# Optimization experiments

Hardware: AMD Instinct MI355X
Metric: run time of the kernel (lower is better)

Reference implementation:

```python
import jax, jax.numpy as jnp
import numpy as np
from jax import lax

NVOX = 100
EPS = 1e-4
DN = ('NDHWC', 'DHWIO', 'NDHWC')

# scn semantics emulated densely: inactive voxels are identically zero and the
# active-site mask is re-applied after every layer, so submanifold convolution,
# strided sparse conv, sparse deconv and masked BN-ReLU compute the same values
# at active sites as SparseConvNet's rulebook gather-GEMM-scatter.

def _bnrelu(x, p, mask):
    # p: [4, C] = (gamma, beta, running_mean, running_var); inference-form BN.
    g, b, mu, v = p[0], p[1], p[2], p[3]
    return jax.nn.relu((x - mu) * (g * lax.rsqrt(v + EPS)) + b) * mask

def _subconv(x, w, mask):
    # Submanifold conv: inputs outside active set are zero; outputs only at active sites.
    return lax.conv_general_dilated(x, w, (1, 1, 1), 'SAME', dimension_numbers=DN) * mask

def _down(x, w):
    # scn.Convolution(dim, a, b, size=2, stride=2, bias=False)
    return lax.conv_general_dilated(x, w, (2, 2, 2), 'VALID', dimension_numbers=DN)

def _up(x, w, mask):
    # scn.Deconvolution restores the pre-downsample active set -> mask with finer mask.
    return lax.conv_transpose(x, w, (2, 2, 2), 'VALID', dimension_numbers=DN) * mask

def _pool_mask(mask):
    return lax.reduce_window(mask, 0.0, lax.max, (1, 2, 2, 2, 1), (1, 2, 2, 2, 1), 'VALID')

def _forward(coords, feats, w_in, w0a, wdown0, w1a, wdown1, w2, wup1, w1post, wup0, w0post,
             bnA, bnB, bnC, bnD, bnE, bnF, bnG, bnH, bnI, bnJ, linW, linb):
    i, j, k = coords[:, 0], coords[:, 1], coords[:, 2]
    # InputLayer mode=3: sum features at duplicate coordinates.
    grid = jnp.zeros((1, NVOX, NVOX, NVOX, 1), feats.dtype).at[0, i, j, k, 0].add(feats[:, 0])
    mask0 = jnp.zeros((1, NVOX, NVOX, NVOX, 1), feats.dtype).at[0, i, j, k, 0].set(1.0)
    mask1 = _pool_mask(mask0)   # 50^3 active set after strided conv
    mask2 = _pool_mask(mask1)   # 25^3

    x = _subconv(grid, w_in, mask0)                          # 1 -> 32
    x0 = _subconv(_bnrelu(x, bnA, mask0), w0a, mask0)        # level-0 VGG block
    d0 = _down(_bnrelu(x0, bnB, mask0), wdown0)              # 32 -> 64, 100 -> 50
    x1 = _subconv(_bnrelu(d0, bnC, mask1), w1a, mask1)       # level-1 VGG block
    d1 = _down(_bnrelu(x1, bnD, mask1), wdown1)              # 64 -> 96, 50 -> 25
    x2 = _subconv(_bnrelu(d1, bnE, mask2), w2, mask2)        # level-2 VGG block
    u1 = _up(_bnrelu(x2, bnF, mask2), wup1, mask1)           # 96 -> 64, 25 -> 50
    y1 = _subconv(_bnrelu(jnp.concatenate([x1, u1], -1), bnG, mask1), w1post, mask1)  # 128 -> 64
    u0 = _up(_bnrelu(y1, bnH, mask1), wup0, mask0)           # 64 -> 32, 50 -> 100
    y0 = _subconv(_bnrelu(jnp.concatenate([x0, u0], -1), bnI, mask0), w0post, mask0)  # 64 -> 32
    y = _bnrelu(y0, bnJ, mask0)                              # final BatchNormReLU(32)
    pts = y[0, i, j, k, :]                                   # OutputLayer: gather active sites [N,32]
    return pts @ linW + linb                                 # Linear(32, 3)


def setup_inputs() -> dict:
    key = jax.random.key(0)
    ks = jax.random.split(key, 24)
    N = 120000
    coords = jax.random.randint(ks[0], (N, 3), 0, NVOX, dtype=jnp.int32)
    feats = jax.random.normal(ks[1], (N, 1), jnp.float32)

    def w(k, shape, fan_in):
        return (jax.random.normal(k, shape, jnp.float32) / np.float32(np.sqrt(fan_in)))

    def bn(k, c):
        k1, k2, k3, k4 = jax.random.split(k, 4)
        return jnp.stack([
            1.0 + 0.1 * jax.random.normal(k1, (c,)),
            0.1 * jax.random.normal(k2, (c,)),
            0.1 * jax.random.normal(k3, (c,)),
            0.5 + jax.random.uniform(k4, (c,)),
        ]).astype(jnp.float32)

    return dict(
        coords=coords, feats=feats,
        w_in=w(ks[2], (3, 3, 3, 1, 32), 27),
        w0a=w(ks[3], (3, 3, 3, 32, 32), 27 * 32),
        wdown0=w(ks[4], (2, 2, 2, 32, 64), 8 * 32),
        w1a=w(ks[5], (3, 3, 3, 64, 64), 27 * 64),
        wdown1=w(ks[6], (2, 2, 2, 64, 96), 8 * 64),
        w2=w(ks[7], (3, 3, 3, 96, 96), 27 * 96),
        wup1=w(ks[8], (2, 2, 2, 96, 64), 96),
        w1post=w(ks[9], (3, 3, 3, 128, 64), 27 * 128),
        wup0=w(ks[10], (2, 2, 2, 64, 32), 64),
        w0post=w(ks[11], (3, 3, 3, 64, 32), 27 * 64),
        bnA=bn(ks[12], 32), bnB=bn(ks[13], 32), bnC=bn(ks[14], 64), bnD=bn(ks[15], 64),
        bnE=bn(ks[16], 96), bnF=bn(ks[17], 96), bnG=bn(ks[18], 128), bnH=bn(ks[19], 64),
        bnI=bn(ks[20], 64), bnJ=bn(ks[21], 32),
        linW=w(ks[22], (32, 3), 32),
        linb=0.01 * jax.random.normal(ks[23], (3,), jnp.float32),
    )


def reference(coords, feats, w_in, w0a, wdown0, w1a, wdown1, w2, wup1, w1post, wup0, w0post,
              bnA, bnB, bnC, bnD, bnE, bnF, bnG, bnH, bnI, bnJ, linW, linb):
    return _forward(coords, feats, w_in, w0a, wdown0, w1a, wdown1, w2, wup1, w1post, wup0, w0post,
                    bnA, bnB, bnC, bnD, bnE, bnF, bnG, bnH, bnI, bnJ, linW, linb)
```

## Files before the change

### kernel.cpp

```cpp
#include <hip/hip_runtime.h>


#define NVOX 100
#define EPSB 1e-4f
typedef unsigned long long u64;
typedef _Float16 h2 __attribute__((ext_vector_type(2)));
typedef _Float16 h8 __attribute__((ext_vector_type(8)));
typedef float f16v __attribute__((ext_vector_type(16)));
#define DEVFN __device__ __forceinline__

template<int NTAPS, int CTOT, int COUT>
__global__ __launch_bounds__(256)
void prepB32(const float* __restrict__ w, h2* __restrict__ out)
{
    constexpr int CTG = COUT / 32, KCH = CTOT / 16;
    const int n = NTAPS * CTG * KCH * 256;
    const int idx = blockIdx.x * 256 + threadIdx.x;
    if (idx >= n) return;
    const int jh = idx & 3;
    const int lane = (idx >> 2) & 63;
    int r = idx >> 8;
    const int kc = r % KCH; r /= KCH;
    const int ct = r % CTG; const int t = r / CTG;
    const int k0 = kc * 16 + (lane >> 5) * 8 + 2 * jh;
    const int co = ct * 32 + (lane & 31);
    h2 v;
    v[0] = (_Float16)w[((size_t)t * CTOT + k0) * COUT + co];
    v[1] = (_Float16)w[((size_t)t * CTOT + k0 + 1) * COUT + co];
    out[idx] = v;
}

template<int KC1, int KC2, int CTILES, int COUT, int S>
__global__ __launch_bounds__(64)
void gconv_m32(const h2* __restrict__ inA, const h2* __restrict__ inB,
               const h2* __restrict__ wb,
               const int* __restrict__ amap, const int* __restrict__ vlist,
               const int* __restrict__ cnt, int cap, float* __restrict__ out)
{
    constexpr int KCH = KC1 + KC2;
    constexpr int CTG = COUT / 32;
    const int lane = threadIdx.x;
    const int cntv = *cnt;
    const int wbase = blockIdx.x * 32;
    if (wbase >= cntv) return;
    const int ct0 = blockIdx.y * CTILES;
    const int l31 = lane & 31, ksub = lane >> 5;
    const int slot = wbase + l31;
    const bool on = slot < cntv;
    int X = 0, Y = 0, Z = 0;
    if (on) { const int v = vlist[slot]; X = v % S; const int r = v / S; Y = r % S; Z = r / S; }

    auto calc_ns = [&](int t) -> int {
        int ns = cap;
        if (on) {
            const int dz = t / 9 - 1, dy = (t / 3) % 3 - 1, dx = t % 3 - 1;
            const int nz = Z + dz, ny = Y + dy, nx = X + dx;
            if ((unsigned)nz < (unsigned)S && (unsigned)ny < (unsigned)S &&
                (unsigned)nx < (unsigned)S) {
                const int m = amap[(nz * S + ny) * S + nx];
                if (m >= 0) ns = m;
            }
        }
        return ns;
    };

    f16v acc[CTILES];
#pragma unroll
    for (int c = 0; c < CTILES; ++c) acc[c] = (f16v)(0.f);

    int ns = calc_ns(0);
#pragma unroll 1
    for (int t = 0; t < 27; ++t) {
        const int ns_nxt = (t + 1 < 27) ? calc_ns(t + 1) : cap;
        const h2* __restrict__ wt = wb + ((size_t)t * CTG + ct0) * KCH * 256;
#pragma unroll
        for (int kc = 0; kc < KC1; ++kc) {
            const h8 a = *reinterpret_cast<const h8*>(
                inA + (size_t)ns * (KC1 * 8) + kc * 8 + ksub * 4);
#pragma unroll
            for (int ct = 0; ct < CTILES; ++ct) {
                const h8 b = *reinterpret_cast<const h8*>(
                    wt + ((size_t)ct * KCH + kc) * 256 + lane * 4);
                acc[ct] = __builtin_amdgcn_mfma_f32_32x32x16_f16(a, b, acc[ct], 0, 0, 0);
            }
        }
        if constexpr (KC2 > 0) {
#pragma unroll
            for (int kc = 0; kc < KC2; ++kc) {
                const h8 a = *reinterpret_cast<const h8*>(
                    inB + (size_t)ns * (KC2 * 8) + kc * 8 + ksub * 4);
#pragma unroll
                for (int ct = 0; ct < CTILES; ++ct) {
                    const h8 b = *reinterpret_cast<const h8*>(
                        wt + ((size_t)ct * KCH + KC1 + kc) * 256 + lane * 4);
                    acc[ct] = __builtin_amdgcn_mfma_f32_32x32x16_f16(a, b, acc[ct], 0, 0, 0);
                }
            }
        }
        ns = ns_nxt;
    }
#pragma unroll
    for (int ct = 0; ct < CTILES; ++ct)
#pragma unroll
        for (int r = 0; r < 16; ++r) {
            const int row = (r & 3) + 8 * (r >> 2) + 4 * ksub;
            const int srow = wbase + row;
            if (srow < cntv)
                out[(size_t)srow * COUT + (ct0 + ct) * 32 + l31] = acc[ct][r];
        }
}

template<int KCH, int CTILES, int COUT, int SC>
__global__ __launch_bounds__(64)
void dconv_m32(const h2* __restrict__ in, const h2* __restrict__ wb,
               const int* __restrict__ amap_f, const int* __restrict__ vlist_c,
               const int* __restrict__ cnt_c, int capf, float* __restrict__ out)
{
    constexpr int SF = SC * 2;
    constexpr int CTG = COUT / 32;
    const int lane = threadIdx.x;
    const int cntv = *cnt_c;
    const int wbase = blockIdx.x * 32;
    if (wbase >= cntv) return;
    const int ct0 = blockIdx.y * CTILES;
    const int l31 = lane & 31, ksub = lane >> 5;
    const int slot = wbase + l31;
    const bool on = slot < cntv;
    int X = 0, Y = 0, Z = 0;
    if (on) { const int v = vlist_c[slot]; X = v % SC; const int r = v / SC; Y = r % SC; Z = r / SC; }

    auto calc_ns = [&](int t) -> int {
        int ns = capf;
        if (on) {
            const int fz = 2 * Z + ((t >> 2) & 1);
            const int fy = 2 * Y + ((t >> 1) & 1);
            const int fx = 2 * X + (t & 1);
            const int m = amap_f[(fz * SF + fy) * SF + fx];
            if (m >= 0) ns = m;
        }
        return ns;
    };

    f16v acc[CTILES];
#pragma unroll
    for (int c = 0; c < CTILES; ++c) acc[c] = (f16v)(0.f);

    int ns = calc_ns(0);
#pragma unroll 1
    for (int t = 0; t < 8; ++t) {
        const int ns_nxt = (t + 1 < 8) ? calc_ns(t + 1) : capf;
        const h2* __restrict__ wt = wb + ((size_t)t * CTG + ct0) * KCH * 256;
#pragma unroll
        for (int kc = 0; kc < KCH; ++kc) {
            const h8 a = *reinterpret_cast<const h8*>(
                in + (size_t)ns * (KCH * 8) + kc * 8 + ksub * 4);
#pragma unroll
            for (int ct = 0; ct < CTILES; ++ct) {
                const h8 b = *reinterpret_cast<const h8*>(
                    wt + ((size_t)ct * KCH + kc) * 256 + lane * 4);
                acc[ct] = __builtin_amdgcn_mfma_f32_32x32x16_f16(a, b, acc[ct], 0, 0, 0);
            }
        }
        ns = ns_nxt;
    }
#pragma unroll
    for (int ct = 0; ct < CTILES; ++ct)
#pragma unroll
        for (int r = 0; r < 16; ++r) {
            const int row = (r & 3) + 8 * (r >> 2) + 4 * ksub;
            const int srow = wbase + row;
            if (srow < cntv)
                out[(size_t)srow * COUT + (ct0 + ct) * 32 + l31] = acc[ct][r];
        }
}

__global__ __launch_bounds__(256)
void act_h16(const float* __restrict__ src, h2* __restrict__ dst,
             const float* __restrict__ sc, const float* __restrict__ sh,
             const int* __restrict__ cnt, int C)
{
    const int f = (blockIdx.x * 256 + threadIdx.x) * 8;
    if (f >= (*cnt) * C) return;
    const int c0 = f % C;
    const float4 v0 = *reinterpret_cast<const float4*>(src + f);
    const float4 v1 = *reinterpret_cast<const float4*>(src + f + 4);
    const float r[8] = {
        fmaxf(fmaf(v0.x, sc[c0 + 0], sh[c0 + 0]), 0.f),
        fmaxf(fmaf(v0.y, sc[c0 + 1], sh[c0 + 1]), 0.f),
        fmaxf(fmaf(v0.z, sc[c0 + 2], sh[c0 + 2]), 0.f),
        fmaxf(fmaf(v0.w, sc[c0 + 3], sh[c0 + 3]), 0.f),
        fmaxf(fmaf(v1.x, sc[c0 + 4], sh[c0 + 4]), 0.f),
        fmaxf(fmaf(v1.y, sc[c0 + 5], sh[c0 + 5]), 0.f),
        fmaxf(fmaf(v1.z, sc[c0 + 6], sh[c0 + 6]), 0.f),
        fmaxf(fmaf(v1.w, sc[c0 + 7], sh[c0 + 7]), 0.f)};
    union { float4 v; h2 h[4]; } o;
#pragma unroll
    for (int k = 0; k < 4; ++k) {
        h2 p; p[0] = (_Float16)r[2 * k]; p[1] = (_Float16)r[2 * k + 1];
        o.h[k] = p;
    }
    *reinterpret_cast<float4*>(dst + f / 2) = o.v;
}


template<int CTOT, int COUT>
DEVFN void stage_tap(const float* __restrict__ wtap, int cg32,
                     float* __restrict__ lbuf, int wid, int lane)
{
    constexpr int IPW = CTOT / 32;
#pragma unroll
    for (int i = 0; i < IPW; ++i) {
        const int chunk = wid * IPW + i;
        const int f4i = chunk * 64 + lane;
        const int ci = f4i >> 3, sub = f4i & 7;
        const float* g = wtap + ci * COUT + cg32 + sub * 4;
        __builtin_amdgcn_global_load_lds(
            (const __attribute__((address_space(1))) void*)g,
            (__attribute__((address_space(3))) void*)(lbuf + chunk * 256),
            16, 0, 0);
    }
}

template<int CIN>
DEVFN void dorow8(const float* __restrict__ row, const float* __restrict__ wl,
                  float (&acc)[8])
{
#pragma unroll 4
    for (int c0 = 0; c0 < CIN; c0 += 4) {
        const float4 a = *reinterpret_cast<const float4*>(row + c0);
        const float av[4] = {a.x, a.y, a.z, a.w};
#pragma unroll
        for (int j = 0; j < 4; ++j) {
            const float4 w0 = *reinterpret_cast<const float4*>(wl + (c0 + j) * 32);
            const float4 w1 = *reinterpret_cast<const float4*>(wl + (c0 + j) * 32 + 4);
            acc[0] = fmaf(av[j], w0.x, acc[0]);
            acc[1] = fmaf(av[j], w0.y, acc[1]);
            acc[2] = fmaf(av[j], w0.z, acc[2]);
            acc[3] = fmaf(av[j], w0.w, acc[3]);
            acc[4] = fmaf(av[j], w1.x, acc[4]);
            acc[5] = fmaf(av[j], w1.y, acc[5]);
            acc[6] = fmaf(av[j], w1.z, acc[6]);
            acc[7] = fmaf(av[j], w1.w, acc[7]);
        }
    }
}

template<int CIN, int COUT, int SC>
__global__ __launch_bounds__(256)
void uconv_w(const float* __restrict__ in, const float* __restrict__ w,
             const int* __restrict__ amap_f, const int* __restrict__ vlist_c,
             const int* __restrict__ cnt_c, float* __restrict__ out)
{
    constexpr int SF = SC * 2;
    __shared__ float lw[2][CIN * 32];
    const int tid = threadIdx.x, lane = tid & 63, wid = tid >> 6;
    const int cntv = *cnt_c;
    if (blockIdx.x * 64 >= cntv) return;
    const int slot = blockIdx.x * 64 + lane;
    const int cg32 = blockIdx.y * 32;
    const bool on = slot < cntv;
    int X = 0, Y = 0, Z = 0;
    if (on) { const int v = vlist_c[slot]; X = v % SC; const int r = v / SC; Y = r % SC; Z = r / SC; }
    stage_tap<CIN, COUT>(w + (size_t)7 * CIN * COUT, cg32, lw[0], wid, lane);
    __syncthreads();
#pragma unroll 1
    for (int t = 0; t < 8; ++t) {
        if (t + 1 < 8)
            stage_tap<CIN, COUT>(w + (size_t)(6 - t) * CIN * COUT, cg32,
                                 lw[(t + 1) & 1], wid, lane);
        int cs = -1;
        if (on) {
            const int fz = 2 * Z + ((t >> 2) & 1);
            const int fy = 2 * Y + ((t >> 1) & 1);
            const int fx = 2 * X + (t & 1);
            cs = amap_f[(fz * SF + fy) * SF + fx];
        }
        if (cs >= 0) {
            float acc[8];
#pragma unroll
            for (int q = 0; q < 8; ++q) acc[q] = 0.f;
            dorow8<CIN>(in + (size_t)slot * CIN, &lw[t & 1][wid * 8], acc);
            float* __restrict__ op = out + (size_t)cs * COUT + cg32 + wid * 8;
            *reinterpret_cast<float4*>(op) = make_float4(acc[0], acc[1], acc[2], acc[3]);
            *reinterpret_cast<float4*>(op + 4) = make_float4(acc[4], acc[5], acc[6], acc[7]);
        }
        __syncthreads();
    }
}

template<int OSPLIT, int S>
__global__ __launch_bounds__(64 * OSPLIT)
void cin_k(const float* __restrict__ grid, const float* __restrict__ w,
           const int* __restrict__ vlist, const int* __restrict__ cnt,
           float* __restrict__ out)
{
    constexpr int OW = 32 / OSPLIT;
    const int wOff = __builtin_amdgcn_readfirstlane(threadIdx.x >> 6) * OW;
    const int slot = blockIdx.x * 64 + (threadIdx.x & 63);
    if (slot >= *cnt) return;
    const int v = vlist[slot];
    const int x = v % S;
    const int rem = v / S;
    const int y = rem % S;
    const int z = rem / S;
    float acc[OW];
#pragma unroll
    for (int c = 0; c < OW; ++c) acc[c] = 0.f;
#pragma unroll
    for (int t = 0; t < 27; ++t) {
        const int dz = t / 9 - 1, dy = (t / 3) % 3 - 1, dx = t % 3 - 1;
        const int nz = z + dz, ny = y + dy, nx = x + dx;
        if ((unsigned)nz >= (unsigned)S || (unsigned)ny >= (unsigned)S ||
            (unsigned)nx >= (unsigned)S) continue;
        const float val = grid[(nz * S + ny) * S + nx];
        const float* __restrict__ wp = w + t * 32 + wOff;
#pragma unroll
        for (int c = 0; c < OW; ++c) acc[c] = fmaf(val, wp[c], acc[c]);
    }
    float* __restrict__ op = out + (size_t)slot * 32 + wOff;
#pragma unroll
    for (int c = 0; c < OW; ++c) op[c] = acc[c];
}

__global__ __launch_bounds__(256)
void act_k(const float* __restrict__ src, float* __restrict__ dst,
           const float* __restrict__ sc, const float* __restrict__ sh,
           const int* __restrict__ cnt, int C)
{
    const int f = (blockIdx.x * 256 + threadIdx.x) * 4;
    if (f >= (*cnt) * C) return;
    const int c0 = f % C;
    const float4 v = *reinterpret_cast<const float4*>(src + f);
    float4 o;
    o.x = fmaxf(fmaf(v.x, sc[c0 + 0], sh[c0 + 0]), 0.f);
    o.y = fmaxf(fmaf(v.y, sc[c0 + 1], sh[c0 + 1]), 0.f);
    o.z = fmaxf(fmaf(v.z, sc[c0 + 2], sh[c0 + 2]), 0.f);
    o.w = fmaxf(fmaf(v.w, sc[c0 + 3], sh[c0 + 3]), 0.f);
    *reinterpret_cast<float4*>(dst + f) = o;
}

__global__ __launch_bounds__(256)
void final_k(const int* __restrict__ coords, const float* __restrict__ y0,
             const int* __restrict__ amap0, const float* __restrict__ ssJ,
             const float* __restrict__ linW, const float* __restrict__ linb,
             int N, float* __restrict__ outp)
{
    const int n = blockIdx.x * blockDim.x + threadIdx.x;
    if (n >= N) return;
    const int i = coords[3 * n + 0];
    const int j = coords[3 * n + 1];
    const int k = coords[3 * n + 2];
    const int v = (i * NVOX + j) * NVOX + k;
    const int s = amap0[v];
    float a0 = linb[0], a1 = linb[1], a2 = linb[2];
    if (s >= 0) {
        const float* __restrict__ row = y0 + (size_t)s * 32;
#pragma unroll
        for (int c = 0; c < 32; ++c) {
            const float t = fmaxf(fmaf(row[c], ssJ[c], ssJ[32 + c]), 0.f);
            a0 = fmaf(t, linW[c * 3 + 0], a0);
            a1 = fmaf(t, linW[c * 3 + 1], a1);
            a2 = fmaf(t, linW[c * 3 + 2], a2);
        }
    }
    outp[3 * n + 0] = a0;
    outp[3 * n + 1] = a1;
    outp[3 * n + 2] = a2;
}

__global__ void bn_prep(const float* __restrict__ A, const float* __restrict__ B,
                        const float* __restrict__ C, const float* __restrict__ D,
                        const float* __restrict__ E, const float* __restrict__ F,
                        const float* __restrict__ G, const float* __restrict__ H,
                        const float* __restrict__ I, const float* __restrict__ J,
                        float* __restrict__ ss)
{
    const float* bp[10] = {A, B, C, D, E, F, G, H, I, J};
    const int CH[10] = {32, 32, 64, 64, 96, 96, 128, 64, 64, 32};
    int idx = blockIdx.x * blockDim.x + threadIdx.x;
    if (idx >= 672) return;
    int l = 0, base = 0, off2 = 0;
    while (idx >= base + CH[l]) { base += CH[l]; off2 += 2 * CH[l]; ++l; }
    const int c = idx - base;
    const float* bn = bp[l];
    const int Cc = CH[l];
    const float g = bn[c], b = bn[Cc + c], mu = bn[2 * Cc + c], var = bn[3 * Cc + c];
    const float sc = g * rsqrtf(var + EPSB);
    ss[off2 + c] = sc;
    ss[off2 + Cc + c] = b - mu * sc;
}

__global__ __launch_bounds__(256)
void scatter_mark(const int* __restrict__ coords, const float* __restrict__ feats,
                  int N, float* __restrict__ grid, int* __restrict__ amap0)
{
    const int n = blockIdx.x * blockDim.x + threadIdx.x;
    if (n >= N) return;
    const int i = coords[3 * n + 0];
    const int j = coords[3 * n + 1];
    const int k = coords[3 * n + 2];
    const int v = (i * NVOX + j) * NVOX + k;
    atomicAdd(&grid[v], feats[n]);
    amap0[v] = -2;
}

template<int SC>
__global__ __launch_bounds__(256)
void flag_coarse(const int* __restrict__ amap_f, int* __restrict__ amap_c)
{
    constexpr int SF = SC * 2;
    const int v = blockIdx.x * blockDim.x + threadIdx.x;
    if (v >= SC * SC * SC) return;
    const int x = v % SC;
    const int rem = v / SC;
    const int y = rem % SC;
    const int z = rem / SC;
    bool any = false;
#pragma unroll
    for (int t = 0; t < 8; ++t) {
        const int fz = 2 * z + ((t >> 2) & 1);
        const int fy = 2 * y + ((t >> 1) & 1);
        const int fx = 2 * x + (t & 1);
        if (amap_f[(fz * SF + fy) * SF + fx] >= 0) any = true;
    }
    amap_c[v] = any ? -2 : -1;
}

__global__ __launch_bounds__(256)
void count_k(const int* __restrict__ flags, int V, int* __restrict__ counts)
{
    const int v = blockIdx.x * 256 + threadIdx.x;
    const bool act = (v < V) && (flags[v] == -2);
    const u64 m = __ballot(act);
    __shared__ int c[4];
    const int wid = threadIdx.x >> 6;
    if ((threadIdx.x & 63) == 0) c[wid] = __popcll(m);
    __syncthreads();
    if (threadIdx.x == 0) counts[blockIdx.x] = c[0] + c[1] + c[2] + c[3];
}

__global__ __launch_bounds__(1024)
void scan_k(int* __restrict__ counts, int nb, int* __restrict__ total)
{
    __shared__ int sums[1024];
    const int t = threadIdx.x;
    int v[4];
    int s = 0;
#pragma unroll
    for (int i = 0; i < 4; ++i) {
        const int idx = t * 4 + i;
        v[i] = (idx < nb) ? counts[idx] : 0;
        s += v[i];
    }
    sums[t] = s;
    __syncthreads();
    for (int d = 1; d < 1024; d <<= 1) {
        const int add = (t >= d) ? sums[t - d] : 0;
        __syncthreads();
        sums[t] += add;
        __syncthreads();
    }
    int base = (t > 0) ? sums[t - 1] : 0;
#pragma unroll
    for (int i = 0; i < 4; ++i) {
        const int idx = t * 4 + i;
        if (idx < nb) counts[idx] = base;
        base += v[i];
    }
    if (t == 1023) *total = sums[1023];
}

__global__ __launch_bounds__(256)
void emit_k(int* __restrict__ amap, int V, const int* __restrict__ offsets,
            int* __restrict__ vlist)
{
    const int v = blockIdx.x * 256 + threadIdx.x;
    const bool act = (v < V) && (amap[v] == -2);
    const u64 m = __ballot(act);
    __shared__ int wbase[4];
    const int wid = threadIdx.x >> 6;
    const int lane = threadIdx.x & 63;
    if (lane == 0) wbase[wid] = __popcll(m);
    __syncthreads();
    if (threadIdx.x == 0) {
        int s = 0;
#pragma unroll
        for (int i = 0; i < 4; ++i) { const int t = wbase[i]; wbase[i] = s; s += t; }
    }
    __syncthreads();
    if (act) {
        const int slot = offsets[blockIdx.x] + wbase[wid] +
                         __popcll(m & ((1ull << lane) - 1ull));
        amap[v] = slot;
        vlist[slot] = v;
    }
}

extern "C" void kernel_launch(void* const* d_in, const int* in_sizes, int n_in,
                              void* d_out, int out_size, void* d_ws, size_t ws_size,
                              hipStream_t stream) {
    const int*   coords = (const int*)d_in[0];
    const float* feats  = (const float*)d_in[1];
    const float* w_in   = (const float*)d_in[2];
    const float* w0a    = (const float*)d_in[3];
    const float* wdown0 = (const float*)d_in[4];
    const float* w1a    = (const float*)d_in[5];
    const float* wdown1 = (const float*)d_in[6];
    const float* w2     = (const float*)d_in[7];
    const float* wup1   = (const float*)d_in[8];
    const float* w1post = (const float*)d_in[9];
    const float* wup0   = (const float*)d_in[10];
    const float* w0post = (const float*)d_in[11];
    const float* linW = (const float*)d_in[22];
    const float* linb = (const float*)d_in[23];
    float* outp = (float*)d_out;

    const int N = in_sizes[1];
    const int V0 = NVOX * NVOX * NVOX;
    const int V1 = 50 * 50 * 50;
    const int V2 = 25 * 25 * 25;
    const int cap0 = N;
    const int cap1 = 100000;
    const int cap2 = V2;

    char* ws = (char*)d_ws;
    size_t off = 0;
    auto alloc = [&](size_t bytes) -> void* {
        void* p = ws + off;
        off += (bytes + 255) & ~(size_t)255;
        return p;
    };
    int*   amap0  = (int*)alloc((size_t)V0 * 4);
    int*   vlist0 = (int*)alloc((size_t)cap0 * 4);
    int*   amap1  = (int*)alloc((size_t)V1 * 4);
    int*   vlist1 = (int*)alloc((size_t)cap1 * 4);
    int*   amap2  = (int*)alloc((size_t)V2 * 4);
    int*   vlist2 = (int*)alloc((size_t)cap2 * 4);
    int*   cnt    = (int*)alloc(3 * 4);
    int*   counts = (int*)alloc(4096 * 4);
    float* ss     = (float*)alloc(1344 * 4);
    float* grid   = (float*)alloc((size_t)V0 * 4);
    float* P1 = (float*)alloc((size_t)cap0 * 32 * 4);
    float* P2 = (float*)alloc((size_t)cap0 * 32 * 4);
    float* P3 = (float*)alloc((size_t)cap0 * 32 * 4);
    float* Q1 = (float*)alloc((size_t)cap1 * 64 * 4);
    float* Q2 = (float*)alloc((size_t)cap1 * 64 * 4);
    float* Q3 = (float*)alloc((size_t)cap1 * 64 * 4);
    float* R1 = (float*)alloc((size_t)cap2 * 96 * 4);
    float* R2 = (float*)alloc((size_t)cap2 * 96 * 4);
    h2* wbA  = (h2*)alloc((size_t)27 * 1 * 2 * 256 * 4);
    h2* wb1  = (h2*)alloc((size_t)27 * 2 * 4 * 256 * 4);
    h2* wb2  = (h2*)alloc((size_t)27 * 3 * 6 * 256 * 4);
    h2* wbP1 = (h2*)alloc((size_t)27 * 2 * 8 * 256 * 4);
    h2* wbP0 = (h2*)alloc((size_t)27 * 1 * 4 * 256 * 4);
    h2* wbD0 = (h2*)alloc((size_t)8 * 2 * 2 * 256 * 4);
    h2* wbD1 = (h2*)alloc((size_t)8 * 3 * 4 * 256 * 4);
    if (off > ws_size) return;

    h2* HA  = (h2*)P3;
    h2* HB  = (h2*)P3;
    h2* HC  = (h2*)Q3;
    h2* HD  = (h2*)Q3;
    h2* HE  = (h2*)Q1;
    h2* HG1 = (h2*)Q3;
    h2* HG2 = (h2*)P1;
    h2* HI1 = (h2*)P3;
    h2* HI2 = (h2*)Q2;

    const int B = 256;
    const int gN  = (N + B - 1) / B;
    const int nb0 = (V0 + B - 1) / B;
    const int nb1 = (V1 + B - 1) / B;
    const int nb2 = (V2 + B - 1) / B;
    const int gA64 = (cap1 * 64 / 4 + 255) / 256;
    const int gA96 = (cap2 * 96 / 4 + 255) / 256;
    const int gH32_0 = (cap0 * 32 / 8 + 255) / 256;
    const int gH64_1 = (cap1 * 64 / 8 + 255) / 256;
    const int gH96_2 = (cap2 * 96 / 8 + 255) / 256;
    const int sb0 = (cap0 + 63) / 64;
    const int sb1 = (cap1 + 63) / 64;
    const int sb2 = (cap2 + 63) / 64;
    const int g1w_0 = (cap0 + 31) / 32;
    const int g1w_1 = (cap1 + 31) / 32;
    const int g1w_2 = (cap2 + 31) / 32;

    hipMemsetAsync(amap0, 0xFF, (size_t)V0 * 4, stream);
    hipMemsetAsync(grid, 0, (size_t)V0 * 4, stream);
    bn_prep<<<3, 256, 0, stream>>>((const float*)d_in[12], (const float*)d_in[13],
                                   (const float*)d_in[14], (const float*)d_in[15],
                                   (const float*)d_in[16], (const float*)d_in[17],
                                   (const float*)d_in[18], (const float*)d_in[19],
                                   (const float*)d_in[20], (const float*)d_in[21], ss);
    prepB32<27, 32, 32><<<(27 * 1 * 2 * 256 + 255) / 256, 256, 0, stream>>>(w0a, wbA);
    prepB32<27, 64, 64><<<(27 * 2 * 4 * 256 + 255) / 256, 256, 0, stream>>>(w1a, wb1);
    prepB32<27, 96, 96><<<(27 * 3 * 6 * 256 + 255) / 256, 256, 0, stream>>>(w2, wb2);
    prepB32<27, 128, 64><<<(27 * 2 * 8 * 256 + 255) / 256, 256, 0, stream>>>(w1post, wbP1);
    prepB32<27, 64, 32><<<(27 * 1 * 4 * 256 + 255) / 256, 256, 0, stream>>>(w0post, wbP0);
    prepB32<8, 32, 64><<<(8 * 2 * 2 * 256 + 255) / 256, 256, 0, stream>>>(wdown0, wbD0);
    prepB32<8, 64, 96><<<(8 * 3 * 4 * 256 + 255) / 256, 256, 0, stream>>>(wdown1, wbD1);
    scatter_mark<<<gN, B, 0, stream>>>(coords, feats, N, grid, amap0);
    count_k<<<nb0, B, 0, stream>>>(amap0, V0, counts);
    scan_k<<<1, 1024, 0, stream>>>(counts, nb0, cnt + 0);
    emit_k<<<nb0, B, 0, stream>>>(amap0, V0, counts, vlist0);
    flag_coarse<50><<<nb1, B, 0, stream>>>(amap0, amap1);
    count_k<<<nb1, B, 0, stream>>>(amap1, V1, counts);
    scan_k<<<1, 1024, 0, stream>>>(counts, nb1, cnt + 1);
    emit_k<<<nb1, B, 0, stream>>>(amap1, V1, counts, vlist1);
    flag_coarse<25><<<nb2, B, 0, stream>>>(amap1, amap2);
    count_k<<<nb2, B, 0, stream>>>(amap2, V2, counts);
    scan_k<<<1, 1024, 0, stream>>>(counts, nb2, cnt + 2);
    emit_k<<<nb2, B, 0, stream>>>(amap2, V2, counts, vlist2);

    cin_k<2, 100><<<sb0, 128, 0, stream>>>(grid, w_in, vlist0, cnt + 0, P1);
    act_h16<<<gH32_0, 256, 0, stream>>>(P1, HA, ss + 0, ss + 32, cnt + 0, 32);
    hipMemsetAsync(HA + (size_t)cap0 * 16, 0, 16 * 4, stream);
    gconv_m32<2, 0, 1, 32, 100><<<dim3(g1w_0, 1), 64, 0, stream>>>(
        HA, nullptr, wbA, amap0, vlist0, cnt + 0, cap0, P2);
    act_h16<<<gH32_0, 256, 0, stream>>>(P2, HB, ss + 64, ss + 96, cnt + 0, 32);
    dconv_m32<2, 2, 64, 50><<<dim3(g1w_1, 1), 64, 0, stream>>>(
        HB, wbD0, amap0, vlist1, cnt + 1, cap0, Q1);
    act_h16<<<gH64_1, 256, 0, stream>>>(Q1, HC, ss + 128, ss + 192, cnt + 1, 64);
    hipMemsetAsync(HC + (size_t)cap1 * 32, 0, 32 * 4, stream);
    gconv_m32<4, 0, 2, 64, 50><<<dim3(g1w_1, 1), 64, 0, stream>>>(
        HC, nullptr, wb1, amap1, vlist1, cnt + 1, cap1, Q2);
    act_h16<<<gH64_1, 256, 0, stream>>>(Q2, HD, ss + 256, ss + 320, cnt + 1, 64);
    dconv_m32<4, 1, 96, 25><<<dim3(g1w_2, 3), 64, 0, stream>>>(
        HD, wbD1, amap1, vlist2, cnt + 2, cap1, R1);
    act_h16<<<gH96_2, 256, 0, stream>>>(R1, HE, ss + 384, ss + 480, cnt + 2, 96);
    hipMemsetAsync(HE + (size_t)cap2 * 48, 0, 48 * 4, stream);
    gconv_m32<6, 0, 1, 96, 25><<<dim3(g1w_2, 3), 64, 0, stream>>>(
        HE, nullptr, wb2, amap2, vlist2, cnt + 2, cap2, R2);
    act_k<<<gA96, 256, 0, stream>>>(R2, R2, ss + 576, ss + 672, cnt + 2, 96);
    uconv_w<96, 64, 25><<<dim3(sb2, 2), 256, 0, stream>>>(
        R2, wup1, amap1, vlist2, cnt + 2, Q1);
    act_h16<<<gH64_1, 256, 0, stream>>>(Q2, HG1, ss + 768, ss + 896, cnt + 1, 64);
    hipMemsetAsync(HG1 + (size_t)cap1 * 32, 0, 32 * 4, stream);
    act_h16<<<gH64_1, 256, 0, stream>>>(Q1, HG2, ss + 768 + 64, ss + 896 + 64, cnt + 1, 64);
    hipMemsetAsync(HG2 + (size_t)cap1 * 32, 0, 32 * 4, stream);
    gconv_m32<4, 4, 2, 64, 50><<<dim3(g1w_1, 1), 64, 0, stream>>>(
        HG1, HG2, wbP1, amap1, vlist1, cnt + 1, cap1, Q2);
    act_k<<<gA64, 256, 0, stream>>>(Q2, Q2, ss + 1024, ss + 1088, cnt + 1, 64);
    uconv_w<64, 32, 50><<<dim3(sb1, 1), 256, 0, stream>>>(
        Q2, wup0, amap0, vlist1, cnt + 1, P1);
    act_h16<<<gH32_0, 256, 0, stream>>>(P2, HI1, ss + 1152, ss + 1216, cnt + 0, 32);
    hipMemsetAsync(HI1 + (size_t)cap0 * 16, 0, 16 * 4, stream);
    act_h16<<<gH32_0, 256, 0, stream>>>(P1, HI2, ss + 1152 + 32, ss + 1216 + 32, cnt + 0, 32);
    hipMemsetAsync(HI2 + (size_t)cap0 * 16, 0, 16 * 4, stream);
    gconv_m32<2, 2, 1, 32, 100><<<dim3(g1w_0, 1), 64, 0, stream>>>(
        HI1, HI2, wbP0, amap0, vlist0, cnt + 0, cap0, P2);
    final_k<<<gN, B, 0, stream>>>(coords, P2, amap0, ss + 1280, linW, linb, N, outp);
}
```

Before: 515.8 us.

## Fuse BN-ReLU and fp16 conversion into conv epilogues, drop activation kernels

Folds the inference BatchNorm+ReLU and half-precision conversion into the epilogues of the sparse conv, downsample, upsample and input-conv kernels. Each conv output is written straight as the fp16 activation buffer the next layer reads, or as two differently normalized buffers when a skip connection needs one. This removes the separate act_h16/act_k passes and the fp32 intermediate round trips through memory, and moves the padding-row memsets to the start. Gconv/dconv now use one 32-channel tile per block with more blocks along y, trading weight reuse per block for parallelism. The epilogue now writes scattered 2-byte stores instead of vectorized ones.

```diff
diff --git a/kernel.cpp b/kernel.cpp
--- a/kernel.cpp
+++ b/kernel.cpp
@@ -8,6 +8,8 @@
 typedef _Float16 h8 __attribute__((ext_vector_type(8)));
 typedef float f16v __attribute__((ext_vector_type(16)));
 #define DEVFN __device__ __forceinline__
+
+DEVFN float bnr(float v, float sc, float sh) { return fmaxf(fmaf(v, sc, sh), 0.f); }
 
 template<int NTAPS, int CTOT, int COUT>
 __global__ __launch_bounds__(256)
@@ -30,12 +32,32 @@
     out[idx] = v;
 }
 
-template<int KC1, int KC2, int CTILES, int COUT, int S>
+template<int EMODE, int COUT>
+DEVFN void epilogue(float a, int srow, int ch,
+                    float* outF, _Float16* o1, const float* sc1, const float* sh1,
+                    _Float16* o2, const float* sc2, const float* sh2)
+{
+    if constexpr (EMODE == 0) {
+        outF[(size_t)srow * COUT + ch] = a;
+    } else if constexpr (EMODE == 3) {
+        outF[(size_t)srow * COUT + ch] = bnr(a, sc1[ch], sh1[ch]);
+    } else {
+        o1[(size_t)srow * COUT + ch] = (_Float16)bnr(a, sc1[ch], sh1[ch]);
+        if constexpr (EMODE == 2)
+            o2[(size_t)srow * COUT + ch] = (_Float16)bnr(a, sc2[ch], sh2[ch]);
+    }
+}
+
+template<int KC1, int KC2, int COUT, int S, int EMODE>
 __global__ __launch_bounds__(64)
 void gconv_m32(const h2* __restrict__ inA, const h2* __restrict__ inB,
                const h2* __restrict__ wb,
                const int* __restrict__ amap, const int* __restrict__ vlist,
-               const int* __restrict__ cnt, int cap, float* __restrict__ out)
+               const int* __restrict__ cnt, int cap,
+               float* __restrict__ outF, _Float16* __restrict__ o1,
+               const float* __restrict__ sc1, const float* __restrict__ sh1,
+               _Float16* __restrict__ o2,
+               const float* __restrict__ sc2, const float* __restrict__ sh2)
 {
     constexpr int KCH = KC1 + KC2;
     constexpr int CTG = COUT / 32;
@@ -43,7 +65,7 @@
     const int cntv = *cnt;
     const int wbase = blockIdx.x * 32;
     if (wbase >= cntv) return;
-    const int ct0 = blockIdx.y * CTILES;
+    const int ct0 = blockIdx.y;
     const int l31 = lane & 31, ksub = lane >> 5;
     const int slot = wbase + l31;
     const bool on = slot < cntv;
@@ -64,10 +86,7 @@
         return ns;
     };
 
-    f16v acc[CTILES];
-#pragma unroll
-    for (int c = 0; c < CTILES; ++c) acc[c] = (f16v)(0.f);
-
+    f16v acc = (f16v)(0.f);
     int ns = calc_ns(0);
 #pragma unroll 1
     for (int t = 0; t < 27; ++t) {
@@ -77,44 +96,39 @@
         for (int kc = 0; kc < KC1; ++kc) {
             const h8 a = *reinterpret_cast<const h8*>(
                 inA + (size_t)ns * (KC1 * 8) + kc * 8 + ksub * 4);
-#pragma unroll
-            for (int ct = 0; ct < CTILES; ++ct) {
-                const h8 b = *reinterpret_cast<const h8*>(
-                    wt + ((size_t)ct * KCH + kc) * 256 + lane * 4);
-                acc[ct] = __builtin_amdgcn_mfma_f32_32x32x16_f16(a, b, acc[ct], 0, 0, 0);
-            }
+            const h8 b = *reinterpret_cast<const h8*>(
+                wt + (size_t)kc * 256 + lane * 4);
+            acc = __builtin_amdgcn_mfma_f32_32x32x16_f16(a, b, acc, 0, 0, 0);
         }
         if constexpr (KC2 > 0) {
 #pragma unroll
             for (int kc = 0; kc < KC2; ++kc) {
                 const h8 a = *reinterpret_cast<const h8*>(
                     inB + (size_t)ns * (KC2 * 8) + kc * 8 + ksub * 4);
-#pragma unroll
-                for (int ct = 0; ct < CTILES; ++ct) {
-                    const h8 b = *reinterpret_cast<const h8*>(
-                        wt + ((size_t)ct * KCH + KC1 + kc) * 256 + lane * 4);
-                    acc[ct] = __builtin_amdgcn_mfma_f32_32x32x16_f16(a, b, acc[ct], 0, 0, 0);
-                }
+                const h8 b = *reinterpret_cast<const h8*>(
+                    wt + (size_t)(KC1 + kc) * 256 + lane * 4);
+                acc = __builtin_amdgcn_mfma_f32_32x32x16_f16(a, b, acc, 0, 0, 0);
             }
         }
         ns = ns_nxt;
     }
-#pragma unroll
-    for (int ct = 0; ct < CTILES; ++ct)
-#pragma unroll
-        for (int r = 0; r < 16; ++r) {
-            const int row = (r & 3) + 8 * (r >> 2) + 4 * ksub;
-            const int srow = wbase + row;
-            if (srow < cntv)
-                out[(size_t)srow * COUT + (ct0 + ct) * 32 + l31] = acc[ct][r];
-        }
-}
-
-template<int KCH, int CTILES, int COUT, int SC>
+    const int ch = ct0 * 32 + l31;
+#pragma unroll
+    for (int r = 0; r < 16; ++r) {
+        const int row = (r & 3) + 8 * (r >> 2) + 4 * ksub;
+        const int srow = wbase + row;
+        if (srow < cntv)
+            epilogue<EMODE, COUT>(acc[r], srow, ch, outF, o1, sc1, sh1, o2, sc2, sh2);
+    }
+}
+
+template<int KCH, int COUT, int SC, int EMODE>
 __global__ __launch_bounds__(64)
 void dconv_m32(const h2* __restrict__ in, const h2* __restrict__ wb,
                const int* __restrict__ amap_f, const int* __restrict__ vlist_c,
-               const int* __restrict__ cnt_c, int capf, float* __restrict__ out)
+               const int* __restrict__ cnt_c, int capf,
+               float* __restrict__ outF, _Float16* __restrict__ o1,
+               const float* __restrict__ sc1, const float* __restrict__ sh1)
 {
     constexpr int SF = SC * 2;
     constexpr int CTG = COUT / 32;
@@ -122,7 +136,7 @@
     const int cntv = *cnt_c;
     const int wbase = blockIdx.x * 32;
     if (wbase >= cntv) return;
-    const int ct0 = blockIdx.y * CTILES;
+    const int ct0 = blockIdx.y;
     const int l31 = lane & 31, ksub = lane >> 5;
     const int slot = wbase + l31;
     const bool on = slot < cntv;
@@ -141,10 +155,7 @@
         return ns;
     };
 
-    f16v acc[CTILES];
-#pragma unroll
-    for (int c = 0; c < CTILES; ++c) acc[c] = (f16v)(0.f);
-
+    f16v acc = (f16v)(0.f);
     int ns = calc_ns(0);
 #pragma unroll 1
     for (int t = 0; t < 8; ++t) {
@@ -154,52 +165,21 @@
         for (int kc = 0; kc < KCH; ++kc) {
             const h8 a = *reinterpret_cast<const h8*>(
                 in + (size_t)ns * (KCH * 8) + kc * 8 + ksub * 4);
-#pragma unroll
-            for (int ct = 0; ct < CTILES; ++ct) {
-                const h8 b = *reinterpret_cast<const h8*>(
-                    wt + ((size_t)ct * KCH + kc) * 256 + lane * 4);
-                acc[ct] = __builtin_amdgcn_mfma_f32_32x32x16_f16(a, b, acc[ct], 0, 0, 0);
-            }
+            const h8 b = *reinterpret_cast<const h8*>(
+                wt + (size_t)kc * 256 + lane * 4);
+            acc = __builtin_amdgcn_mfma_f32_32x32x16_f16(a, b, acc, 0, 0, 0);
         }
         ns = ns_nxt;
     }
-#pragma unroll
-    for (int ct = 0; ct < CTILES; ++ct)
-#pragma unroll
-        for (int r = 0; r < 16; ++r) {
-            const int row = (r & 3) + 8 * (r >> 2) + 4 * ksub;
-            const int srow = wbase + row;
-            if (srow < cntv)
-                out[(size_t)srow * COUT + (ct0 + ct) * 32 + l31] = acc[ct][r];
-        }
-}
-
-__global__ __launch_bounds__(256)
-void act_h16(const float* __restrict__ src, h2* __restrict__ dst,
-             const float* __restrict__ sc, const float* __restrict__ sh,
-             const int* __restrict__ cnt, int C)
-{
-    const int f = (blockIdx.x * 256 + threadIdx.x) * 8;
-    if (f >= (*cnt) * C) return;
-    const int c0 = f % C;
-    const float4 v0 = *reinterpret_cast<const float4*>(src + f);
-    const float4 v1 = *reinterpret_cast<const float4*>(src + f + 4);
-    const float r[8] = {
-        fmaxf(fmaf(v0.x, sc[c0 + 0], sh[c0 + 0]), 0.f),
-        fmaxf(fmaf(v0.y, sc[c0 + 1], sh[c0 + 1]), 0.f),
-        fmaxf(fmaf(v0.z, sc[c0 + 2], sh[c0 + 2]), 0.f),
-        fmaxf(fmaf(v0.w, sc[c0 + 3], sh[c0 + 3]), 0.f),
-        fmaxf(fmaf(v1.x, sc[c0 + 4], sh[c0 + 4]), 0.f),
-        fmaxf(fmaf(v1.y, sc[c0 + 5], sh[c0 + 5]), 0.f),
-        fmaxf(fmaf(v1.z, sc[c0 + 6], sh[c0 + 6]), 0.f),
-        fmaxf(fmaf(v1.w, sc[c0 + 7], sh[c0 + 7]), 0.f)};
-    union { float4 v; h2 h[4]; } o;
-#pragma unroll
-    for (int k = 0; k < 4; ++k) {
-        h2 p; p[0] = (_Float16)r[2 * k]; p[1] = (_Float16)r[2 * k + 1];
-        o.h[k] = p;
-    }
-    *reinterpret_cast<float4*>(dst + f / 2) = o.v;
+    const int ch = ct0 * 32 + l31;
+#pragma unroll
+    for (int r = 0; r < 16; ++r) {
+        const int row = (r & 3) + 8 * (r >> 2) + 4 * ksub;
+        const int srow = wbase + row;
+        if (srow < cntv)
+            epilogue<EMODE, COUT>(acc[r], srow, ch, outF, o1, sc1, sh1,
+                                  nullptr, nullptr, nullptr);
+    }
 }
 
 
@@ -249,7 +229,8 @@
 __global__ __launch_bounds__(256)
 void uconv_w(const float* __restrict__ in, const float* __restrict__ w,
              const int* __restrict__ amap_f, const int* __restrict__ vlist_c,
-             const int* __restrict__ cnt_c, float* __restrict__ out)
+             const int* __restrict__ cnt_c, _Float16* __restrict__ out,
+             const float* __restrict__ sc, const float* __restrict__ sh)
 {
     constexpr int SF = SC * 2;
     __shared__ float lw[2][CIN * 32];
@@ -280,22 +261,25 @@
 #pragma unroll
             for (int q = 0; q < 8; ++q) acc[q] = 0.f;
             dorow8<CIN>(in + (size_t)slot * CIN, &lw[t & 1][wid * 8], acc);
-            float* __restrict__ op = out + (size_t)cs * COUT + cg32 + wid * 8;
-            *reinterpret_cast<float4*>(op) = make_float4(acc[0], acc[1], acc[2], acc[3]);
-            *reinterpret_cast<float4*>(op + 4) = make_float4(acc[4], acc[5], acc[6], acc[7]);
+            union { float4 v[1]; _Float16 h[8]; } o;
+            const int chb = cg32 + wid * 8;
+#pragma unroll
+            for (int q = 0; q < 8; ++q)
+                o.h[q] = (_Float16)bnr(acc[q], sc[chb + q], sh[chb + q]);
+            *reinterpret_cast<float4*>(out + (size_t)cs * COUT + chb) = o.v[0];
         }
         __syncthreads();
     }
 }
 
-template<int OSPLIT, int S>
-__global__ __launch_bounds__(64 * OSPLIT)
+template<int S>
+__global__ __launch_bounds__(128)
 void cin_k(const float* __restrict__ grid, const float* __restrict__ w,
            const int* __restrict__ vlist, const int* __restrict__ cnt,
-           float* __restrict__ out)
-{
-    constexpr int OW = 32 / OSPLIT;
-    const int wOff = __builtin_amdgcn_readfirstlane(threadIdx.x >> 6) * OW;
+           _Float16* __restrict__ out, const float* __restrict__ sc,
+           const float* __restrict__ sh)
+{
+    const int wOff = __builtin_amdgcn_readfirstlane(threadIdx.x >> 6) * 16;
     const int slot = blockIdx.x * 64 + (threadIdx.x & 63);
     if (slot >= *cnt) return;
     const int v = vlist[slot];
@@ -303,9 +287,9 @@
     const int rem = v / S;
     const int y = rem % S;
     const int z = rem / S;
-    float acc[OW];
-#pragma unroll
-    for (int c = 0; c < OW; ++c) acc[c] = 0.f;
+    float acc[16];
+#pragma unroll
+    for (int c = 0; c < 16; ++c) acc[c] = 0.f;
 #pragma unroll
     for (int t = 0; t < 27; ++t) {
         const int dz = t / 9 - 1, dy = (t / 3) % 3 - 1, dx = t % 3 - 1;
@@ -315,28 +299,15 @@
         const float val = grid[(nz * S + ny) * S + nx];
         const float* __restrict__ wp = w + t * 32 + wOff;
 #pragma unroll
-        for (int c = 0; c < OW; ++c) acc[c] = fmaf(val, wp[c], acc[c]);
-    }
-    float* __restrict__ op = out + (size_t)slot * 32 + wOff;
-#pragma unroll
-    for (int c = 0; c < OW; ++c) op[c] = acc[c];
-}
-
-__global__ __launch_bounds__(256)
-void act_k(const float* __restrict__ src, float* __restrict__ dst,
-           const float* __restrict__ sc, const float* __restrict__ sh,
-           const int* __restrict__ cnt, int C)
-{
-    const int f = (blockIdx.x * 256 + threadIdx.x) * 4;
-    if (f >= (*cnt) * C) return;
-    const int c0 = f % C;
-    const float4 v = *reinterpret_cast<const float4*>(src + f);
-    float4 o;
-    o.x = fmaxf(fmaf(v.x, sc[c0 + 0], sh[c0 + 0]), 0.f);
-    o.y = fmaxf(fmaf(v.y, sc[c0 + 1], sh[c0 + 1]), 0.f);
-    o.z = fmaxf(fmaf(v.z, sc[c0 + 2], sh[c0 + 2]), 0.f);
-    o.w = fmaxf(fmaf(v.w, sc[c0 + 3], sh[c0 + 3]), 0.f);
-    *reinterpret_cast<float4*>(dst + f) = o;
+        for (int c = 0; c < 16; ++c) acc[c] = fmaf(val, wp[c], acc[c]);
+    }
+    union { float4 v[2]; _Float16 h[16]; } o;
+#pragma unroll
+    for (int c = 0; c < 16; ++c)
+        o.h[c] = (_Float16)bnr(acc[c], sc[wOff + c], sh[wOff + c]);
+    float4* dst = reinterpret_cast<float4*>(out + (size_t)slot * 32 + wOff);
+    dst[0] = o.v[0];
+    dst[1] = o.v[1];
 }
 
 __global__ __launch_bounds__(256)
@@ -357,7 +328,7 @@
         const float* __restrict__ row = y0 + (size_t)s * 32;
 #pragma unroll
         for (int c = 0; c < 32; ++c) {
-            const float t = fmaxf(fmaf(row[c], ssJ[c], ssJ[32 + c]), 0.f);
+            const float t = bnr(row[c], ssJ[c], ssJ[32 + c]);
             a0 = fmaf(t, linW[c * 3 + 0], a0);
             a1 = fmaf(t, linW[c * 3 + 1], a1);
             a2 = fmaf(t, linW[c * 3 + 2], a2);
@@ -540,14 +511,18 @@
     int*   counts = (int*)alloc(4096 * 4);
     float* ss     = (float*)alloc(1344 * 4);
     float* grid   = (float*)alloc((size_t)V0 * 4);
-    float* P1 = (float*)alloc((size_t)cap0 * 32 * 4);
-    float* P2 = (float*)alloc((size_t)cap0 * 32 * 4);
-    float* P3 = (float*)alloc((size_t)cap0 * 32 * 4);
-    float* Q1 = (float*)alloc((size_t)cap1 * 64 * 4);
-    float* Q2 = (float*)alloc((size_t)cap1 * 64 * 4);
-    float* Q3 = (float*)alloc((size_t)cap1 * 64 * 4);
-    float* R1 = (float*)alloc((size_t)cap2 * 96 * 4);
-    float* R2 = (float*)alloc((size_t)cap2 * 96 * 4);
+    _Float16* HA  = (_Float16*)alloc((size_t)(cap0 + 1) * 32 * 2);
+    _Float16* HB  = (_Float16*)alloc((size_t)(cap0 + 1) * 32 * 2);
+    _Float16* HI1 = (_Float16*)alloc((size_t)(cap0 + 1) * 32 * 2);
+    _Float16* HI2 = (_Float16*)alloc((size_t)(cap0 + 1) * 32 * 2);
+    _Float16* HC  = (_Float16*)alloc((size_t)(cap1 + 1) * 64 * 2);
+    _Float16* HD  = (_Float16*)alloc((size_t)(cap1 + 1) * 64 * 2);
+    _Float16* HG1 = (_Float16*)alloc((size_t)(cap1 + 1) * 64 * 2);
+    _Float16* HG2 = (_Float16*)alloc((size_t)(cap1 + 1) * 64 * 2);
+    _Float16* HE  = (_Float16*)alloc((size_t)(cap2 + 1) * 96 * 2);
+    float* y0f  = (float*)alloc((size_t)cap0 * 32 * 4);
+    float* actF = (float*)alloc((size_t)cap2 * 96 * 4);
+    float* actH = (float*)alloc((size_t)cap1 * 64 * 4);
     h2* wbA  = (h2*)alloc((size_t)27 * 1 * 2 * 256 * 4);
     h2* wb1  = (h2*)alloc((size_t)27 * 2 * 4 * 256 * 4);
     h2* wb2  = (h2*)alloc((size_t)27 * 3 * 6 * 256 * 4);
@@ -557,26 +532,11 @@
     h2* wbD1 = (h2*)alloc((size_t)8 * 3 * 4 * 256 * 4);
     if (off > ws_size) return;
 
-    h2* HA  = (h2*)P3;
-    h2* HB  = (h2*)P3;
-    h2* HC  = (h2*)Q3;
-    h2* HD  = (h2*)Q3;
-    h2* HE  = (h2*)Q1;
-    h2* HG1 = (h2*)Q3;
-    h2* HG2 = (h2*)P1;
-    h2* HI1 = (h2*)P3;
-    h2* HI2 = (h2*)Q2;
-
     const int B = 256;
     const int gN  = (N + B - 1) / B;
     const int nb0 = (V0 + B - 1) / B;
     const int nb1 = (V1 + B - 1) / B;
     const int nb2 = (V2 + B - 1) / B;
-    const int gA64 = (cap1 * 64 / 4 + 255) / 256;
-    const int gA96 = (cap2 * 96 / 4 + 255) / 256;
-    const int gH32_0 = (cap0 * 32 / 8 + 255) / 256;
-    const int gH64_1 = (cap1 * 64 / 8 + 255) / 256;
-    const int gH96_2 = (cap2 * 96 / 8 + 255) / 256;
     const int sb0 = (cap0 + 63) / 64;
     const int sb1 = (cap1 + 63) / 64;
     const int sb2 = (cap2 + 63) / 64;
@@ -586,6 +546,15 @@
 
     hipMemsetAsync(amap0, 0xFF, (size_t)V0 * 4, stream);
     hipMemsetAsync(grid, 0, (size_t)V0 * 4, stream);
+    hipMemsetAsync(HA + (size_t)cap0 * 32, 0, 64, stream);
+    hipMemsetAsync(HB + (size_t)cap0 * 32, 0, 64, stream);
+    hipMemsetAsync(HI1 + (size_t)cap0 * 32, 0, 64, stream);
+    hipMemsetAsync(HI2 + (size_t)cap0 * 32, 0, 64, stream);
+    hipMemsetAsync(HC + (size_t)cap1 * 64, 0, 128, stream);
+    hipMemsetAsync(HD + (size_t)cap1 * 64, 0, 128, stream);
+    hipMemsetAsync(HG1 + (size_t)cap1 * 64, 0, 128, stream);
+    hipMemsetAsync(HG2 + (size_t)cap1 * 64, 0, 128, stream);
+    hipMemsetAsync(HE + (size_t)cap2 * 96, 0, 192, stream);
     bn_prep<<<3, 256, 0, stream>>>((const float*)d_in[12], (const float*)d_in[13],
                                    (const float*)d_in[14], (const float*)d_in[15],
                                    (const float*)d_in[16], (const float*)d_in[17],
@@ -611,42 +580,32 @@
     scan_k<<<1, 1024, 0, stream>>>(counts, nb2, cnt + 2);
     emit_k<<<nb2, B, 0, stream>>>(amap2, V2, counts, vlist2);
 
-    cin_k<2, 100><<<sb0, 128, 0, stream>>>(grid, w_in, vlist0, cnt + 0, P1);
-    act_h16<<<gH32_0, 256, 0, stream>>>(P1, HA, ss + 0, ss + 32, cnt + 0, 32);
-    hipMemsetAsync(HA + (size_t)cap0 * 16, 0, 16 * 4, stream);
-    gconv_m32<2, 0, 1, 32, 100><<<dim3(g1w_0, 1), 64, 0, stream>>>(
-        HA, nullptr, wbA, amap0, vlist0, cnt + 0, cap0, P2);
-    act_h16<<<gH32_0, 256, 0, stream>>>(P2, HB, ss + 64, ss + 96, cnt + 0, 32);
-    dconv_m32<2, 2, 64, 50><<<dim3(g1w_1, 1), 64, 0, stream>>>(
-        HB, wbD0, amap0, vlist1, cnt + 1, cap0, Q1);
-    act_h16<<<gH64_1, 256, 0, stream>>>(Q1, HC, ss + 128, ss + 192, cnt + 1, 64);
-    hipMemsetAsync(HC + (size_t)cap1 * 32, 0, 32 * 4, stream);
-    gconv_m32<4, 0, 2, 64, 50><<<dim3(g1w_1, 1), 64, 0, stream>>>(
-        HC, nullptr, wb1, amap1, vlist1, cnt + 1, cap1, Q2);
-    act_h16<<<gH64_1, 256, 0, stream>>>(Q2, HD, ss + 256, ss + 320, cnt + 1, 64);
-    dconv_m32<4, 1, 96, 25><<<dim3(g1w_2, 3), 64, 0, stream>>>(
-        HD, wbD1, amap1, vlist2, cnt + 2, cap1, R1);
-    act_h16<<<gH96_2, 256, 0, stream>>>(R1, HE, ss + 384, ss + 480, cnt + 2, 96);
-    hipMemsetAsync(HE + (size_t)cap2 * 48, 0, 48 * 4, stream);
-    gconv_m32<6, 0, 1, 96, 25><<<dim3(g1w_2, 3), 64, 0, stream>>>(
-        HE, nullptr, wb2, amap2, vlist2, cnt + 2, cap2, R2);
-    act_k<<<gA96, 256, 0, stream>>>(R2, R2, ss + 576, ss + 672, cnt + 2, 96);
+    cin_k<100><<<sb0, 128, 0, stream>>>(grid, w_in, vlist0, cnt + 0, HA,
+                                        ss + 0, ss + 32);
+    gconv_m32<2, 0, 32, 100, 2><<<dim3(g1w_0, 1), 64, 0, stream>>>(
+        (const h2*)HA, nullptr, wbA, amap0, vlist0, cnt + 0, cap0,
+        nullptr, HB, ss + 64, ss + 96, HI1, ss + 1152, ss + 1216);
+    dconv_m32<2, 64, 50, 1><<<dim3(g1w_1, 2), 64, 0, stream>>>(
+        (const h2*)HB, wbD0, amap0, vlist1, cnt + 1, cap0,
+        nullptr, HC, ss + 128, ss + 192);
+    gconv_m32<4, 0, 64, 50, 2><<<dim3(g1w_1, 2), 64, 0, stream>>>(
+        (const h2*)HC, nullptr, wb1, amap1, vlist1, cnt + 1, cap1,
+        nullptr, HD, ss + 256, ss + 320, HG1, ss + 768, ss + 896);
+    dconv_m32<4, 96, 25, 1><<<dim3(g1w_2, 3), 64, 0, stream>>>(
+        (const h2*)HD, wbD1, amap1, vlist2, cnt + 2, cap1,
+        nullptr, HE, ss + 384, ss + 480);
+    gconv_m32<6, 0, 96, 25, 3><<<dim3(g1w_2, 3), 64, 0, stream>>>(
+        (const h2*)HE, nullptr, wb2, amap2, vlist2, cnt + 2, cap2,
+        actF, nullptr, ss + 576, ss + 672, nullptr, nullptr, nullptr);
     uconv_w<96, 64, 25><<<dim3(sb2, 2), 256, 0, stream>>>(
-        R2, wup1, amap1, vlist2, cnt + 2, Q1);
-    act_h16<<<gH64_1, 256, 0, stream>>>(Q2, HG1, ss + 768, ss + 896, cnt + 1, 64);
-    hipMemsetAsync(HG1 + (size_t)cap1 * 32, 0, 32 * 4, stream);
-    act_h16<<<gH64_1, 256, 0, stream>>>(Q1, HG2, ss + 768 + 64, ss + 896 + 64, cnt + 1, 64);
-    hipMemsetAsync(HG2 + (size_t)cap1 * 32, 0, 32 * 4, stream);
-    gconv_m32<4, 4, 2, 64, 50><<<dim3(g1w_1, 1), 64, 0, stream>>>(
-        HG1, HG2, wbP1, amap1, vlist1, cnt + 1, cap1, Q2);
-    act_k<<<gA64, 256, 0, stream>>>(Q2, Q2, ss + 1024, ss + 1088, cnt + 1, 64);
+        actF, wup1, amap1, vlist2, cnt + 2, HG2, ss + 768 + 64, ss + 896 + 64);
+    gconv_m32<4, 4, 64, 50, 3><<<dim3(g1w_1, 2), 64, 0, stream>>>(
+        (const h2*)HG1, (const h2*)HG2, wbP1, amap1, vlist1, cnt + 1, cap1,
+        actH, nullptr, ss + 1024, ss + 1088, nullptr, nullptr, nullptr);
     uconv_w<64, 32, 50><<<dim3(sb1, 1), 256, 0, stream>>>(
-        Q2, wup0, amap0, vlist1, cnt + 1, P1);
-    act_h16<<<gH32_0, 256, 0, stream>>>(P2, HI1, ss + 1152, ss + 1216, cnt + 0, 32);
-    hipMemsetAsync(HI1 + (size_t)cap0 * 16, 0, 16 * 4, stream);
-    act_h16<<<gH32_0, 256, 0, stream>>>(P1, HI2, ss + 1152 + 32, ss + 1216 + 32, cnt + 0, 32);
-    hipMemsetAsync(HI2 + (size_t)cap0 * 16, 0, 16 * 4, stream);
-    gconv_m32<2, 2, 1, 32, 100><<<dim3(g1w_0, 1), 64, 0, stream>>>(
-        HI1, HI2, wbP0, amap0, vlist0, cnt + 0, cap0, P2);
-    final_k<<<gN, B, 0, stream>>>(coords, P2, amap0, ss + 1280, linW, linb, N, outp);
-}
+        actH, wup0, amap0, vlist1, cnt + 1, HI2, ss + 1152 + 32, ss + 1216 + 32);
+    gconv_m32<2, 2, 32, 100, 0><<<dim3(g1w_0, 1), 64, 0, stream>>>(
+        (const h2*)HI1, (const h2*)HI2, wbP0, amap0, vlist0, cnt + 0, cap0,
+        y0f, nullptr, nullptr, nullptr, nullptr, nullptr, nullptr);
+    final_k<<<gN, B, 0, stream>>>(coords, y0f, amap0, ss + 1280, linW, linb, N, outp);
+}
```

Result: slower. 552.8 us (+7.2%).
